# Kernel optimization log

Hardware: AMD Instinct MI355X
Metric: run time of the kernel (lower is better)

Reference implementation:

```python
import jax, jax.numpy as jnp
import numpy as np

DN = ('NCDHW', 'OIDHW', 'NCDHW')


def conv3d(x, w, b, stride=2, pad=1):
    # w: [Cout, Cin, k, k, k] (PyTorch Conv3d layout == OIDHW)
    y = jax.lax.conv_general_dilated(x, w, (stride,) * 3, [(pad, pad)] * 3,
                                     dimension_numbers=DN)
    return y + b[None, :, None, None, None]


def convT3d(x, w, b, stride=2, pad=1):
    # w: [Cin, Cout, k, k, k] (PyTorch ConvTranspose3d layout).
    # ConvTranspose(k,s,p) == conv(lhs_dilated by s, flipped kernel, pad = k-1-p)
    k = w.shape[2]
    wf = jnp.transpose(jnp.flip(w, (2, 3, 4)), (1, 0, 2, 3, 4))  # -> OIDHW
    p = k - 1 - pad
    y = jax.lax.conv_general_dilated(x, wf, (1, 1, 1), [(p, p)] * 3,
                                     lhs_dilation=(stride,) * 3,
                                     dimension_numbers=DN)
    return y + b[None, :, None, None, None]


def setup_inputs() -> dict:
    key = jax.random.key(0)
    ks = jax.random.split(key, 14)
    s = 0.05
    inp = {
        'x': jax.random.normal(ks[0], (4, 1, 128, 128, 128), jnp.float32),
        # encoder conv weights (OIDHW) + biases
        'w1': jax.random.normal(ks[1], (16, 1, 4, 4, 4), jnp.float32) * s,
        'b1': jnp.zeros((16,), jnp.float32),
        'w2': jax.random.normal(ks[2], (32, 16, 4, 4, 4), jnp.float32) * s,
        'b2': jnp.zeros((32,), jnp.float32),
        'w3': jax.random.normal(ks[3], (64, 32, 4, 4, 4), jnp.float32) * s,
        'b3': jnp.zeros((64,), jnp.float32),
        # VQ codebook [num_embeddings=512, latent_dim=64]
        'codebook': jax.random.normal(ks[4], (512, 64), jnp.float32),
        # decoder conv-transpose weights (PyTorch layout: [Cin, Cout, k,k,k]) + biases
        'dw1': jax.random.normal(ks[5], (64, 32, 4, 4, 4), jnp.float32) * s,
        'db1': jnp.zeros((32,), jnp.float32),
        'dw2': jax.random.normal(ks[6], (32, 16, 4, 4, 4), jnp.float32) * s,
        'db2': jnp.zeros((16,), jnp.float32),
        'dw3': jax.random.normal(ks[7], (16, 1, 4, 4, 4), jnp.float32) * s,
        'db3': jnp.zeros((1,), jnp.float32),
    }
    return inp


def reference(x, w1, b1, w2, b2, w3, b3, codebook, dw1, db1, dw2, db2, dw3, db3):
    # ---- encoder ----
    h = jax.nn.relu(conv3d(x, w1, b1))
    h = jax.nn.relu(conv3d(h, w2, b2))
    z_e = conv3d(h, w3, b3)                      # [B, C=64, D, H, W]
    B, C, D, H, W = z_e.shape

    # ---- vector quantization (cdist + argmin + gather) ----
    zf = jnp.transpose(z_e.reshape(B, C, -1), (0, 2, 1))   # [B, N, C]
    # squared euclidean distances (argmin identical to cdist argmin)
    d2 = (jnp.sum(zf * zf, axis=-1, keepdims=True)
          + jnp.sum(codebook * codebook, axis=-1)[None, None, :]
          - 2.0 * jnp.einsum('bnc,kc->bnk', zf, codebook))  # [B, N, K]
    encoding_indices = jnp.argmin(d2, axis=-1)              # [B, N]
    q = codebook[encoding_indices]                          # [B, N, C]
    quantized = jnp.transpose(q, (0, 2, 1)).reshape(B, C, D, H, W)
    # straight-through estimator
    quantized = z_e + jax.lax.stop_gradient(quantized - z_e)

    # ---- decoder ----
    h = jax.nn.relu(convT3d(quantized, dw1, db1))
    h = jax.nn.relu(convT3d(h, dw2, db2))
    x_hat = jax.nn.sigmoid(convT3d(h, dw3, db3))
    return (x_hat, quantized, z_e)
```

## Files before the change

### kernel.cpp

```cpp
#include <hip/hip_runtime.h>
#include <math.h>


__device__ __forceinline__ float4 ld4(const float* p) {
  float4 q; __builtin_memcpy(&q, p, 16); return q;
}
struct F3 { float x, y, z; };
__device__ __forceinline__ F3 ld3(const float* p) {
  F3 q; __builtin_memcpy(&q, p, 12); return q;
}

#define WAVES_HINT __attribute__((amdgpu_waves_per_eu(2, 4)))

template<int CIN, int COUT>
__global__ __launch_bounds__(256) void k_repackT(const float* __restrict__ w,
                                                 float* __restrict__ dst) {
  const int idx = blockIdx.x * 256 + threadIdx.x;
  if (idx >= CIN * 8 * COUT * 8) return;
  const int a  = idx & 7;
  const int co = (idx >> 3) % COUT;
  const int p  = ((idx >> 3) / COUT) & 7;
  const int ci2 = idx / (8 * COUT * 8);
  const int az = a >> 2, ay = (a >> 1) & 1, ax = a & 1;
  const int pz = p >> 2, py = (p >> 1) & 1, px = p & 1;
  const int kz = 3 - pz - 2 * az, ky = 3 - py - 2 * ay, kx = 3 - px - 2 * ax;
  dst[(((size_t)(ci2 * 8 + p) * COUT + co) * 16) + az * 8 + (ay * 2 + ax)] =
      w[((size_t)ci2 * COUT + co) * 64 + (kz * 16 + ky * 4 + kx)];
}

template<int S, int D, int NCH>
__global__ __launch_bounds__(256) void k_zhalo(float* __restrict__ buf) {
  const int vol = S * S * S;
  const long long idx = (long long)blockIdx.x * 256 + threadIdx.x;
  if (idx >= (long long)NCH * vol) return;
  const int r = (int)(idx % vol);
  const int z = r / (S * S), y = (r / S) % S, x = r % S;
  if (z < 1 || z > D || y < 1 || y > D || x < 1 || x > D) buf[idx] = 0.0f;
}

__global__ __launch_bounds__(256) void k_pad(const float* __restrict__ x,
                                             float* __restrict__ dp) {
  constexpr long long VOL = 130LL * 130 * 130;
  const long long idx = (long long)blockIdx.x * 256 + threadIdx.x;
  if (idx >= 4 * VOL) return;
  const int b = (int)(idx / VOL);
  const int r = (int)(idx % VOL);
  const int z = r / (130 * 130), y = (r / 130) % 130, xx = r % 130;
  float v = 0.0f;
  if (z >= 1 && z <= 128 && y >= 1 && y <= 128 && xx >= 1 && xx <= 128)
    v = x[(((long long)b * 128 + (z - 1)) * 128 + (y - 1)) * 128 + (xx - 1)];
  dp[idx] = v;
}

template<int CIN, int COUT, int DIN, int DOUT, int OCG, int TZ, bool RELU,
         bool INP, int SIN, bool OUTP, int SOUT, int NG>
__global__ __launch_bounds__(256) WAVES_HINT
void k_conv(const float* __restrict__ xin, const float* __restrict__ wg,
            const float* __restrict__ bias, float* __restrict__ out) {
  constexpr int NBX = DOUT / 8, NBY = DOUT / 8, NBZ = DOUT / (4 * TZ);
  constexpr int NWG = 4 * NG * NBX * NBY * NBZ;
  static_assert(NWG % 8 == 0, "bijective XCD swizzle needs NWG%8==0");
  constexpr size_t VIN  = INP  ? (size_t)SIN * SIN * SIN : (size_t)DIN * DIN * DIN;
  constexpr size_t VOUT = OUTP ? (size_t)SOUT * SOUT * SOUT : (size_t)DOUT * DOUT * DOUT;
  const int tid = threadIdx.x;
  const int tx = tid & 7, ty = (tid >> 3) & 7, tz = tid >> 6;
  const int bid = blockIdx.x;
  int bb = (bid & 7) * (NWG / 8) + (bid >> 3);
  const int g  = bb % NG;  bb /= NG;
  const int gx = bb % NBX; bb /= NBX;
  const int gy = bb % NBY; bb /= NBY;
  const int gz = bb % NBZ; bb /= NBZ;
  const int b = bb;
  const int oc0 = g * OCG;
  const int ow = gx * 8 + tx, oh = gy * 8 + ty, od0 = gz * (4 * TZ) + tz;

  float acc[TZ][OCG];
#pragma unroll
  for (int j = 0; j < TZ; ++j)
#pragma unroll
    for (int c = 0; c < OCG; ++c) acc[j][c] = 0.0f;

#pragma unroll 1
  for (int ci = 0; ci < CIN; ++ci) {
    const float* xb = xin + (size_t)(b * CIN + ci) * VIN;
#pragma unroll 1
    for (int t16 = 0; t16 < 16; ++t16) {
      float4 q[TZ];
      if (INP) {
        const int zp = od0 * 2 + (t16 >> 2);
        const int yp = oh * 2 + (t16 & 3);
        const float* r0 = xb + ((size_t)zp * SIN + yp) * SIN + ow * 2;
#pragma unroll
        for (int j = 0; j < TZ; ++j) q[j] = ld4(r0 + (size_t)j * 8 * SIN * SIN);
      } else {
        const int y  = oh * 2 - 1 + (t16 & 3);
        const int x0 = ow * 2 - 1;
        const bool vy = (unsigned)y < (unsigned)DIN;
#pragma unroll
        for (int j = 0; j < TZ; ++j) {
          const int z = od0 * 2 - 1 + (t16 >> 2) + j * 8;
          const bool vz = vy && ((unsigned)z < (unsigned)DIN);
          const float* xr = xb + ((size_t)z * DIN + y) * DIN + x0;
          q[j].x = (vz && (unsigned)(x0 + 0) < (unsigned)DIN) ? xr[0] : 0.0f;
          q[j].y = (vz && (unsigned)(x0 + 1) < (unsigned)DIN) ? xr[1] : 0.0f;
          q[j].z = (vz && (unsigned)(x0 + 2) < (unsigned)DIN) ? xr[2] : 0.0f;
          q[j].w = (vz && (unsigned)(x0 + 3) < (unsigned)DIN) ? xr[3] : 0.0f;
        }
      }
#pragma unroll
      for (int c = 0; c < OCG; ++c) {
        const float4 w4 = ld4(wg + ((size_t)(oc0 + c) * CIN + ci) * 64 + t16 * 4);
#pragma unroll
        for (int j = 0; j < TZ; ++j) {
          acc[j][c] = fmaf(q[j].x, w4.x, acc[j][c]);
          acc[j][c] = fmaf(q[j].y, w4.y, acc[j][c]);
          acc[j][c] = fmaf(q[j].z, w4.z, acc[j][c]);
          acc[j][c] = fmaf(q[j].w, w4.w, acc[j][c]);
        }
      }
    }
  }

#pragma unroll
  for (int c = 0; c < OCG; ++c) {
    const float bv = bias[oc0 + c];
#pragma unroll
    for (int j = 0; j < TZ; ++j) {
      float v = acc[j][c] + bv;
      if (RELU) v = fmaxf(v, 0.0f);
      const int od = od0 + j * 4;
      if (OUTP)
        out[(size_t)(b * COUT + oc0 + c) * VOUT
            + ((size_t)(od + 1) * SOUT + (oh + 1)) * SOUT + (ow + 1)] = v;
      else
        out[(size_t)(b * COUT + oc0 + c) * VOUT
            + ((size_t)od * DOUT + oh) * DOUT + ow] = v;
    }
  }
}

template<int CIN, int COUT, int DIN, int OCG, int TZ, int EPI, int SIN,
         bool OUTP, int SOUT, int NG>
__global__ __launch_bounds__(256) WAVES_HINT
void k_convt(const float* __restrict__ xin, const float* __restrict__ wp,
             const float* __restrict__ bias, float* __restrict__ out) {
  constexpr int DOUT = 2 * DIN, NBX = DIN / 8, NBY = DIN / 8,
                NBZ = DIN / (4 * TZ);
  constexpr int NWG = 4 * NG * NBX * NBY * NBZ;
  static_assert(NWG % 8 == 0, "bijective XCD swizzle needs NWG%8==0");
  constexpr size_t VIN  = (size_t)SIN * SIN * SIN;
  constexpr size_t VOUT = OUTP ? (size_t)SOUT * SOUT * SOUT
                               : (size_t)DOUT * DOUT * DOUT;
  const int tid = threadIdx.x;
  const int tx = tid & 7, ty = (tid >> 3) & 7, tz = tid >> 6;
  const int bid = blockIdx.x;
  int bb = (bid & 7) * (NWG / 8) + (bid >> 3);
  const int g  = bb % NG;  bb /= NG;
  const int gx = bb % NBX; bb /= NBX;
  const int gy = bb % NBY; bb /= NBY;
  const int gz = bb % NBZ; bb /= NBZ;
  const int b = bb;
  const int oc0 = g * OCG;
  const int mx = gx * 8 + tx, my = gy * 8 + ty;
  const int mz0 = gz * (4 * TZ) + tz * TZ;

  float acc[TZ][8][OCG];
#pragma unroll
  for (int j = 0; j < TZ; ++j)
#pragma unroll
    for (int p = 0; p < 8; ++p)
#pragma unroll
      for (int c = 0; c < OCG; ++c) acc[j][p][c] = 0.0f;

#pragma unroll 1
  for (int ci = 0; ci < CIN; ++ci) {
    const float* xb = xin + (size_t)(b * CIN + ci) * VIN
                          + ((size_t)mz0 * SIN + my) * SIN + mx;
    float xn[TZ + 2][3][3];
#pragma unroll
    for (int dz = 0; dz < TZ + 2; ++dz)
#pragma unroll
      for (int dy = 0; dy < 3; ++dy) {
        const F3 t = ld3(xb + ((size_t)dz * SIN + dy) * SIN);
        xn[dz][dy][0] = t.x; xn[dz][dy][1] = t.y; xn[dz][dy][2] = t.z;
      }
    __builtin_amdgcn_sched_barrier(0);

    const float* wci = wp + (size_t)ci * 8 * COUT * 16;
#pragma unroll
    for (int p = 0; p < 8; ++p) {
      const int pz = p >> 2, py = (p >> 1) & 1, px = p & 1;
#pragma unroll
      for (int c = 0; c < OCG; ++c) {
        const float* wb = wci + ((size_t)p * COUT + (oc0 + c)) * 16;
        const float4 wA = ld4(wb);
        const float4 wB = ld4(wb + 8);
#pragma unroll
        for (int j = 0; j < TZ; ++j)
          acc[j][p][c] = fmaf(xn[j + pz][py    ][px    ], wA.x, acc[j][p][c]);
#pragma unroll
        for (int j = 0; j < TZ; ++j)
          acc[j][p][c] = fmaf(xn[j + pz][py    ][px + 1], wA.y, acc[j][p][c]);
#pragma unroll
        for (int j = 0; j < TZ; ++j)
          acc[j][p][c] = fmaf(xn[j + pz][py + 1][px    ], wA.z, acc[j][p][c]);
#pragma unroll
        for (int j = 0; j < TZ; ++j)
          acc[j][p][c] = fmaf(xn[j + pz][py + 1][px + 1], wA.w, acc[j][p][c]);
#pragma unroll
        for (int j = 0; j < TZ; ++j)
          acc[j][p][c] = fmaf(xn[j + pz + 1][py    ][px    ], wB.x, acc[j][p][c]);
#pragma unroll
        for (int j = 0; j < TZ; ++j)
          acc[j][p][c] = fmaf(xn[j + pz + 1][py    ][px + 1], wB.y, acc[j][p][c]);
#pragma unroll
        for (int j = 0; j < TZ; ++j)
          acc[j][p][c] = fmaf(xn[j + pz + 1][py + 1][px    ], wB.z, acc[j][p][c]);
#pragma unroll
        for (int j = 0; j < TZ; ++j)
          acc[j][p][c] = fmaf(xn[j + pz + 1][py + 1][px + 1], wB.w, acc[j][p][c]);
      }
    }
  }

#pragma unroll
  for (int c = 0; c < OCG; ++c) {
    const float bv = bias[oc0 + c];
#pragma unroll
    for (int j = 0; j < TZ; ++j) {
      const int mz = mz0 + j;
#pragma unroll
      for (int p = 0; p < 8; ++p) {
        const int pz = p >> 2, py = (p >> 1) & 1, px = p & 1;
        float v = acc[j][p][c] + bv;
        if (EPI == 1) v = fmaxf(v, 0.0f);
        if (EPI == 2) v = 1.0f / (1.0f + expf(-v));
        if (OUTP)
          out[(size_t)(b * COUT + oc0 + c) * VOUT
              + ((size_t)(2 * mz + pz + 1) * SOUT + (2 * my + py + 1)) * SOUT
              + (2 * mx + px + 1)] = v;
        else
          out[(size_t)(b * COUT + oc0 + c) * VOUT
              + ((size_t)(2 * mz + pz) * DOUT + (2 * my + py)) * DOUT
              + (2 * mx + px)] = v;
      }
    }
  }
}

__global__ __launch_bounds__(256) void k_vq(const float* __restrict__ ze,
                                            const float* __restrict__ cb,
                                            float* __restrict__ quant,
                                            float* __restrict__ quantp) {
  __shared__ float ct[64 * 65];
  __shared__ float zs[4][64];
  __shared__ int   bis[4];
  const int tid  = threadIdx.x;
  const int lane = tid & 63;
  const int wv   = tid >> 6;
  const int p0 = blockIdx.x * 4;
  const int b  = p0 >> 12;
  const int n0 = p0 & 4095;

  {
    const int c = tid >> 2, j = tid & 3;
    zs[j][c] = ze[((size_t)(b * 64 + c) << 12) + n0 + j];
  }

  float best = 3.4e38f;
  int bi = 0;
#pragma unroll 1
  for (int ch = 0; ch < 8; ++ch) {
    __syncthreads();
    for (int i = tid; i < 4096; i += 256) {
      const int r = i >> 6, c = i & 63;
      ct[r * 65 + c] = cb[((ch * 64 + r) << 6) + c];
    }
    __syncthreads();
    float d = 0.0f;
#pragma unroll 8
    for (int c = 0; c < 64; ++c) {
      const float t = zs[wv][c] - ct[lane * 65 + c];
      d = fmaf(t, t, d);
    }
    const int k = ch * 64 + lane;
    if (d < best) { best = d; bi = k; }
  }
#pragma unroll
  for (int off = 32; off > 0; off >>= 1) {
    const float ob = __shfl_down(best, off);
    const int   oi = __shfl_down(bi, off);
    if (ob < best || (ob == best && oi < bi)) { best = ob; bi = oi; }
  }
  if (lane == 0) bis[wv] = bi;
  __syncthreads();
  {
    const int c = tid >> 2, j = tid & 3;
    const float val = cb[(bis[j] << 6) + c];
    const int n = n0 + j;
    quant[((size_t)(b * 64 + c) << 12) + n] = val;
    const int zz = n >> 8, yy = (n >> 4) & 15, xx = n & 15;
    quantp[(size_t)(b * 64 + c) * 8000
           + ((size_t)(zz + 1) * 20 + (yy + 1)) * 20 + (xx + 1)] = val;
  }
}

extern "C" void kernel_launch(void* const* d_in, const int* in_sizes, int n_in,
                              void* d_out, int out_size, void* d_ws, size_t ws_size,
                              hipStream_t stream) {
  const float* x   = (const float*)d_in[0];
  const float* w1  = (const float*)d_in[1];
  const float* b1  = (const float*)d_in[2];
  const float* w2  = (const float*)d_in[3];
  const float* b2  = (const float*)d_in[4];
  const float* w3  = (const float*)d_in[5];
  const float* b3  = (const float*)d_in[6];
  const float* cb  = (const float*)d_in[7];
  const float* dw1 = (const float*)d_in[8];
  const float* db1 = (const float*)d_in[9];
  const float* dw2 = (const float*)d_in[10];
  const float* db2 = (const float*)d_in[11];
  const float* dw3 = (const float*)d_in[12];
  const float* db3 = (const float*)d_in[13];

  float* outf  = (float*)d_out;
  float* xhat  = outf;
  float* quant = outf + 8388608;
  float* ze    = outf + 9437184;

  float* dp = outf;

  float* regA = (float*)d_ws;
  float* regB = regA + (size_t)64 * 68 * 68 * 68;
  float* regC = regB + (size_t)128 * 36 * 36 * 36;
  float* t1p = regC + (size_t)256 * 20 * 20 * 20;
  float* t2p = t1p + 262144;
  float* t3p = t2p + 65536;

  k_repackT<64, 32><<<512, 256, 0, stream>>>(dw1, t1p);
  k_repackT<32, 16><<<128, 256, 0, stream>>>(dw2, t2p);
  k_repackT<16, 1><<<4, 256, 0, stream>>>(dw3, t3p);
  k_zhalo<68, 64, 64><<<78608, 256, 0, stream>>>(regA);
  k_zhalo<36, 32, 128><<<23328, 256, 0, stream>>>(regB);
  k_zhalo<20, 16, 256><<<8000, 256, 0, stream>>>(regC);
  k_pad<<<34329, 256, 0, stream>>>(x, dp);

  k_conv<1, 16, 128, 64, 16, 2, true, true, 130, true, 68, 1>
      <<<2048, 256, 0, stream>>>(dp, w1, b1, regA);
  k_conv<16, 32, 64, 32, 16, 1, true, true, 68, true, 36, 2>
      <<<1024, 256, 0, stream>>>(regA, w2, b2, regB);
  k_conv<32, 64, 32, 16, 4, 1, false, true, 36, false, 16, 16>
      <<<1024, 256, 0, stream>>>(regB, w3, b3, ze);
  k_vq<<<4096, 256, 0, stream>>>(ze, cb, quant, regC);
  k_convt<64, 32, 16, 2, 1, 1, 20, true, 36, 16>
      <<<1024, 256, 0, stream>>>(regC, t1p, db1, regB);
  k_convt<32, 16, 32, 2, 2, 1, 36, true, 68, 8>
      <<<2048, 256, 0, stream>>>(regB, t2p, db2, regA);
  k_convt<16, 1, 64, 1, 4, 2, 68, false, 0, 1>
      <<<1024, 256, 0, stream>>>(regA, t3p, db3, xhat);
}
```

Baseline: 983.9 us.

## Stage encoder conv input tiles in LDS with double-buffered channel prefetch

The strided encoder convolution now cooperatively loads an 18x18x(8*TZ+2) input halo tile per block into shared memory. Each thread then reads its 4-wide windows from LDS instead of issuing overlapping global loads. For multi-channel inputs, the next channel's tile is prefetched into registers while the current one is being computed, using two LDS buffers and two barriers per channel. The unpadded-input fallback is removed, so every caller must now pass a padded input. This adds LDS pressure and synchronisation, which may lower occupancy.

```diff
diff --git a/kernel.cpp b/kernel.cpp
--- a/kernel.cpp
+++ b/kernel.cpp
@@ -4,10 +4,17 @@
 
 __device__ __forceinline__ float4 ld4(const float* p) {
   float4 q; __builtin_memcpy(&q, p, 16); return q;
+}
+struct F2 { float x, y; };
+__device__ __forceinline__ F2 ld2(const float* p) {
+  F2 q; __builtin_memcpy(&q, p, 8); return q;
 }
 struct F3 { float x, y, z; };
 __device__ __forceinline__ F3 ld3(const float* p) {
   F3 q; __builtin_memcpy(&q, p, 12); return q;
+}
+__device__ __forceinline__ float4 ldl4(const float* p) {
+  float4 q; __builtin_memcpy(&q, p, 16); return q;
 }
 
 #define WAVES_HINT __attribute__((amdgpu_waves_per_eu(2, 4)))
@@ -60,8 +67,15 @@
   constexpr int NBX = DOUT / 8, NBY = DOUT / 8, NBZ = DOUT / (4 * TZ);
   constexpr int NWG = 4 * NG * NBX * NBY * NBZ;
   static_assert(NWG % 8 == 0, "bijective XCD swizzle needs NWG%8==0");
-  constexpr size_t VIN  = INP  ? (size_t)SIN * SIN * SIN : (size_t)DIN * DIN * DIN;
+  constexpr size_t VIN  = (size_t)SIN * SIN * SIN;
   constexpr size_t VOUT = OUTP ? (size_t)SOUT * SOUT * SOUT : (size_t)DOUT * DOUT * DOUT;
+  constexpr int XT = 18, YT = 18, ZT = 8 * TZ + 2, XTP = 20;
+  constexpr int NF2 = ZT * YT * (XT / 2);
+  constexpr int NR  = (NF2 + 255) / 256;
+  constexpr int NBUF = (CIN > 1) ? 2 : 1;
+  constexpr int TVOL = ZT * YT * XTP;
+  __shared__ float lds[NBUF][ZT][YT][XTP];
+
   const int tid = threadIdx.x;
   const int tx = tid & 7, ty = (tid >> 3) & 7, tz = tid >> 6;
   const int bid = blockIdx.x;
@@ -74,42 +88,40 @@
   const int oc0 = g * OCG;
   const int ow = gx * 8 + tx, oh = gy * 8 + ty, od0 = gz * (4 * TZ) + tz;
 
+  const int x0 = gx * 16, y0 = gy * 16, z0 = gz * (8 * TZ);
+  const float* xt0 = xin + (size_t)b * CIN * VIN
+                   + ((size_t)z0 * SIN + y0) * SIN + x0;
+  float* ldsf = &lds[0][0][0][0];
+
   float acc[TZ][OCG];
 #pragma unroll
   for (int j = 0; j < TZ; ++j)
 #pragma unroll
     for (int c = 0; c < OCG; ++c) acc[j][c] = 0.0f;
 
-#pragma unroll 1
-  for (int ci = 0; ci < CIN; ++ci) {
-    const float* xb = xin + (size_t)(b * CIN + ci) * VIN;
+  if constexpr (CIN == 1) {
+    for (int e = tid; e < NF2; e += 256) {
+      const int ez = e / (YT * (XT / 2));
+      const int rem = e - ez * (YT * (XT / 2));
+      const int ey = rem / (XT / 2);
+      const int m  = rem - ey * (XT / 2);
+      const F2 v = ld2(xt0 + ((size_t)ez * SIN + ey) * SIN + 2 * m);
+      *(F2*)&lds[0][ez][ey][2 * m] = v;
+    }
+    __syncthreads();
+
 #pragma unroll 1
     for (int t16 = 0; t16 < 16; ++t16) {
+      const int dy = t16 & 3, dz = t16 >> 2;
       float4 q[TZ];
-      if (INP) {
-        const int zp = od0 * 2 + (t16 >> 2);
-        const int yp = oh * 2 + (t16 & 3);
-        const float* r0 = xb + ((size_t)zp * SIN + yp) * SIN + ow * 2;
-#pragma unroll
-        for (int j = 0; j < TZ; ++j) q[j] = ld4(r0 + (size_t)j * 8 * SIN * SIN);
-      } else {
-        const int y  = oh * 2 - 1 + (t16 & 3);
-        const int x0 = ow * 2 - 1;
-        const bool vy = (unsigned)y < (unsigned)DIN;
-#pragma unroll
-        for (int j = 0; j < TZ; ++j) {
-          const int z = od0 * 2 - 1 + (t16 >> 2) + j * 8;
-          const bool vz = vy && ((unsigned)z < (unsigned)DIN);
-          const float* xr = xb + ((size_t)z * DIN + y) * DIN + x0;
-          q[j].x = (vz && (unsigned)(x0 + 0) < (unsigned)DIN) ? xr[0] : 0.0f;
-          q[j].y = (vz && (unsigned)(x0 + 1) < (unsigned)DIN) ? xr[1] : 0.0f;
-          q[j].z = (vz && (unsigned)(x0 + 2) < (unsigned)DIN) ? xr[2] : 0.0f;
-          q[j].w = (vz && (unsigned)(x0 + 3) < (unsigned)DIN) ? xr[3] : 0.0f;
-        }
+#pragma unroll
+      for (int j = 0; j < TZ; ++j) {
+        const int zp = (tz + 4 * j) * 2 + dz;
+        q[j] = ldl4(&lds[0][zp][2 * ty + dy][2 * tx]);
       }
 #pragma unroll
       for (int c = 0; c < OCG; ++c) {
-        const float4 w4 = ld4(wg + ((size_t)(oc0 + c) * CIN + ci) * 64 + t16 * 4);
+        const float4 w4 = ld4(wg + (size_t)(oc0 + c) * 64 + t16 * 4);
 #pragma unroll
         for (int j = 0; j < TZ; ++j) {
           acc[j][c] = fmaf(q[j].x, w4.x, acc[j][c]);
@@ -118,6 +130,72 @@
           acc[j][c] = fmaf(q[j].w, w4.w, acc[j][c]);
         }
       }
+    }
+  } else {
+    int goff[NR], loff[NR];
+#pragma unroll
+    for (int r = 0; r < NR; ++r) {
+      const int e = tid + 256 * r;
+      const int ez = e / (YT * (XT / 2));
+      const int rem = e - ez * (YT * (XT / 2));
+      const int ey = rem / (XT / 2);
+      const int m  = rem - ey * (XT / 2);
+      goff[r] = (ez * SIN + ey) * SIN + 2 * m;
+      loff[r] = (ez * YT + ey) * XTP + 2 * m;
+    }
+
+#pragma unroll
+    for (int r = 0; r < NR; ++r)
+      if (tid + 256 * r < NF2) {
+        const F2 v = ld2(xt0 + goff[r]);
+        *(F2*)&ldsf[loff[r]] = v;
+      }
+    __syncthreads();
+
+#pragma unroll 1
+    for (int ci = 0; ci < CIN; ++ci) {
+      F2 rg[NR];
+      const bool pf = (ci + 1 < CIN);
+      if (pf) {
+        const float* xc = xt0 + (size_t)(ci + 1) * VIN;
+#pragma unroll
+        for (int r = 0; r < NR; ++r)
+          if (tid + 256 * r < NF2) rg[r] = ld2(xc + goff[r]);
+      }
+      const int cur = ci & 1;
+      const float* Lb = ldsf + cur * TVOL;
+
+#pragma unroll 1
+      for (int t16 = 0; t16 < 16; ++t16) {
+        const int dy = t16 & 3, dz = t16 >> 2;
+        float4 q[TZ];
+#pragma unroll
+        for (int j = 0; j < TZ; ++j) {
+          const int zp = (tz + 4 * j) * 2 + dz;
+          q[j] = ldl4(Lb + ((size_t)zp * YT + (2 * ty + dy)) * XTP + 2 * tx);
+        }
+#pragma unroll
+        for (int c = 0; c < OCG; ++c) {
+          const float4 w4 =
+              ld4(wg + ((size_t)(oc0 + c) * CIN + ci) * 64 + t16 * 4);
+#pragma unroll
+          for (int j = 0; j < TZ; ++j) {
+            acc[j][c] = fmaf(q[j].x, w4.x, acc[j][c]);
+            acc[j][c] = fmaf(q[j].y, w4.y, acc[j][c]);
+            acc[j][c] = fmaf(q[j].z, w4.z, acc[j][c]);
+            acc[j][c] = fmaf(q[j].w, w4.w, acc[j][c]);
+          }
+        }
+      }
+
+      __syncthreads();
+      if (pf) {
+        float* Ln = ldsf + (cur ^ 1) * TVOL;
+#pragma unroll
+        for (int r = 0; r < NR; ++r)
+          if (tid + 256 * r < NF2) *(F2*)&Ln[loff[r]] = rg[r];
+      }
+      __syncthreads();
     }
   }
 
```

Result: no change. 968.3 us (-1.6%).
